# Kernel optimization log

Measured on AMD Instinct MI355X. Metric: run time of the kernel, lower is better.

Reference implementation:

```python
import jax, jax.numpy as jnp
import numpy as np

B, S, E = 2, 2048, 2048
H, KVH, D = 16, 4, 128
GROUPS = H // KVH
WINDOW = 1024
CAP = 50.0
ROPE_BASE = 10000.0
RMS_EPS = 1e-6
LN_EPS = 1e-5

def setup_inputs() -> dict:
    key = jax.random.key(0)
    ks = jax.random.split(key, 5)
    return {
        "x": jax.random.normal(ks[0], (B, S, E), jnp.float32),
        "Wq": jax.random.normal(ks[1], (E, E), jnp.float32) * (1.0 / np.sqrt(E)),
        "Wk": jax.random.normal(ks[2], (KVH * D, E), jnp.float32) * (1.0 / np.sqrt(E)),
        "Wv": jax.random.normal(ks[3], (KVH * D, E), jnp.float32) * (1.0 / np.sqrt(E)),
        "Wo": jax.random.normal(ks[4], (E, E), jnp.float32) * (1.0 / np.sqrt(E * H)),
        "q_norm_w": jnp.ones((D,), jnp.float32),
        "k_norm_w": jnp.ones((D,), jnp.float32),
        "ln_gamma": jnp.ones((E,), jnp.float32),
        "ln_beta": jnp.zeros((E,), jnp.float32),
    }

def _rmsnorm(t, w):
    # normalize over last (head) dim
    var = jnp.mean(jnp.square(t), axis=-1, keepdims=True)
    return t * jax.lax.rsqrt(var + RMS_EPS) * w

def _rope(t):
    # t: [B, h, S, D]; rotate-half RoPE
    half = D // 2
    inv_freq = 1.0 / (ROPE_BASE ** (jnp.arange(0, D, 2, dtype=jnp.float32) / D))  # [D/2]
    ang = jnp.arange(S, dtype=jnp.float32)[:, None] * inv_freq[None, :]  # [S, D/2]
    cos = jnp.concatenate([jnp.cos(ang), jnp.cos(ang)], axis=-1)  # [S, D]
    sin = jnp.concatenate([jnp.sin(ang), jnp.sin(ang)], axis=-1)
    t1, t2 = t[..., :half], t[..., half:]
    rot = jnp.concatenate([-t2, t1], axis=-1)
    return t * cos + rot * sin

def reference(x, Wq, Wk, Wv, Wo, q_norm_w, k_norm_w, ln_gamma, ln_beta):
    b, s, _ = x.shape
    q = (x @ Wq.T).reshape(b, s, H, D).transpose(0, 2, 1, 3)    # [B,H,S,D]
    k = (x @ Wk.T).reshape(b, s, KVH, D).transpose(0, 2, 1, 3)  # [B,KVH,S,D]
    v = (x @ Wv.T).reshape(b, s, KVH, D).transpose(0, 2, 1, 3)
    # QK-RMSNorm (Gemma/PaLM2 style), then RoPE
    q = _rope(_rmsnorm(q, q_norm_w))
    k = _rope(_rmsnorm(k, k_norm_w))
    # GQA: repeat KV heads to match query heads
    k = jnp.repeat(k, GROUPS, axis=1)  # [B,H,S,D]
    v = jnp.repeat(v, GROUPS, axis=1)
    scores = jnp.einsum('bhqd,bhkd->bhqk', q, k) / jnp.sqrt(jnp.asarray(D, x.dtype))
    # tanh logit softcap (Gemma2)
    scores = CAP * jnp.tanh(scores / CAP)
    # causal + sliding-window mask: attend to j with 0 <= i-j < WINDOW
    i = jnp.arange(s)[:, None]
    j = jnp.arange(s)[None, :]
    mask = (j <= i) & ((i - j) < WINDOW)  # [S,S]
    neg = jnp.finfo(scores.dtype).min
    scores = jnp.where(mask[None, None], scores, neg)
    attn = jax.nn.softmax(scores, axis=-1)
    out = jnp.einsum('bhqk,bhkd->bhqd', attn, v)  # [B,H,S,D]
    out = out.transpose(0, 2, 1, 3).reshape(b, s, E) @ Wo.T
    # residual + LayerNorm (post-norm)
    y = x + out
    mu = jnp.mean(y, axis=-1, keepdims=True)
    var = jnp.var(y, axis=-1, keepdims=True)
    return (y - mu) * jax.lax.rsqrt(var + LN_EPS) * ln_gamma + ln_beta
```

## Files before the change

### kernel.cpp

```cpp
#include <hip/hip_runtime.h>
#include <stdint.h>

typedef __attribute__((ext_vector_type(8))) short short8;
typedef __attribute__((ext_vector_type(4))) float f32x4;
typedef unsigned short u16;
typedef unsigned int u32;

#define NTOK 4096
#define E 2048
#define S 2048
#define NH 16
#define NKVH 4
#define HD 128
#define NQKV 3072

__device__ __forceinline__ float bf2f(u16 u) {
    return __uint_as_float(((u32)u) << 16);
}
__device__ __forceinline__ u16 f2bf(float f) {
    u32 u = __float_as_uint(f);
    u32 r = (u + 0x7fffu + ((u >> 16) & 1u)) >> 16;
    return (u16)r;
}
__device__ __forceinline__ void gload_lds16(const u16* g, u16* l) {
    __builtin_amdgcn_global_load_lds(
        (const __attribute__((address_space(1))) unsigned int*)(g),
        (__attribute__((address_space(3))) unsigned int*)(l), 16, 0, 0);
}

__global__ void cast5(const float* __restrict__ x, const float* __restrict__ wq,
                      const float* __restrict__ wk, const float* __restrict__ wv,
                      const float* __restrict__ wo,
                      u16* __restrict__ xb, u16* __restrict__ wqkvb,
                      u16* __restrict__ wob) {
    int i = blockIdx.x * 256 + threadIdx.x;
    const float* s; u16* d; int rel;
    if (i < 2097152)      { s = x;  d = xb;  rel = i; }
    else if (i < 3145728) { s = wq; d = wqkvb; rel = i - 2097152; }
    else if (i < 3407872) { s = wk; d = wqkvb + 4194304; rel = i - 3145728; }
    else if (i < 3670016) { s = wv; d = wqkvb + 5242880; rel = i - 3407872; }
    else                  { s = wo; d = wob; rel = i - 3670016; }
    float4 v = *(const float4*)(s + (size_t)rel * 4);
    ushort4 o;
    o.x = f2bf(v.x); o.y = f2bf(v.y); o.z = f2bf(v.z); o.w = f2bf(v.w);
    *(ushort4*)(d + (size_t)rel * 4) = o;
}

#define TM 128
#define TN 128
#define BK 64

__global__ __launch_bounds__(256, 3)
void gemm_bt(const u16* __restrict__ A, const u16* __restrict__ Bt, float* __restrict__ C,
             int M, int N, int K) {
    __shared__ u16 As[TM * BK];
    __shared__ u16 Bs[TN * BK];
    const int m0 = blockIdx.y * TM;
    const int n0 = blockIdx.x * TN;
    const int tid = threadIdx.x;
    const int w = tid >> 6, lane = tid & 63;
    const int wm = (w >> 1) * 64, wn = (w & 1) * 64;
    const int lr = lane & 15, quad = lane >> 4;

    f32x4 acc[4][4];
#pragma unroll
    for (int mi = 0; mi < 4; mi++)
#pragma unroll
        for (int ni = 0; ni < 4; ni++)
            acc[mi][ni] = (f32x4){0.f, 0.f, 0.f, 0.f};

    const int srow = w * 8 + (lane >> 3);
    const int scol = (lane & 7) * 8;
    const u16* ga0 = A + (size_t)(m0 + srow) * K + scol;
    const u16* gb0 = Bt + (size_t)(n0 + srow) * K + scol;

    for (int kt = 0; kt < K; kt += BK) {
        __syncthreads();
#pragma unroll
        for (int i = 0; i < 4; i++) {
            gload_lds16(ga0 + (size_t)(i * 32) * K + kt, &As[(w * 8 + i * 32) * BK]);
            gload_lds16(gb0 + (size_t)(i * 32) * K + kt, &Bs[(w * 8 + i * 32) * BK]);
        }
        __syncthreads();
#pragma unroll
        for (int kk = 0; kk < BK; kk += 32) {
            const int ko = kk + quad * 8;
            short8 af[4], bfr[4];
#pragma unroll
            for (int mi = 0; mi < 4; mi++)
                af[mi] = *(const short8*)(&As[(wm + mi * 16 + lr) * BK + ko]);
#pragma unroll
            for (int ni = 0; ni < 4; ni++)
                bfr[ni] = *(const short8*)(&Bs[(wn + ni * 16 + lr) * BK + ko]);
#pragma unroll
            for (int mi = 0; mi < 4; mi++)
#pragma unroll
                for (int ni = 0; ni < 4; ni++)
                    acc[mi][ni] = __builtin_amdgcn_mfma_f32_16x16x32_bf16(
                        af[mi], bfr[ni], acc[mi][ni], 0, 0, 0);
        }
    }
#pragma unroll
    for (int mi = 0; mi < 4; mi++)
#pragma unroll
        for (int ni = 0; ni < 4; ni++) {
            int row = m0 + wm + mi * 16 + quad * 4;
            int col = n0 + wn + ni * 16 + lr;
            f32x4 v = acc[mi][ni];
            C[(size_t)(row + 0) * N + col] = v[0];
            C[(size_t)(row + 1) * N + col] = v[1];
            C[(size_t)(row + 2) * N + col] = v[2];
            C[(size_t)(row + 3) * N + col] = v[3];
        }
}

__global__ __launch_bounds__(256)
void rmsrope2(const float* __restrict__ qkv,
              const float* __restrict__ qw, const float* __restrict__ kw,
              u16* __restrict__ qdst, u16* __restrict__ kdst) {
    int p = blockIdx.x * 4 + (threadIdx.x >> 6);
    int lane = threadIdx.x & 63;
    const float* src; const float* w; u16* dst; int HH;
    if (p < NTOK * NH) { src = qkv; w = qw; dst = qdst; HH = NH; }
    else { p -= NTOK * NH; src = qkv + 2048; w = kw; dst = kdst; HH = NKVH; }
    int n = p / HH;
    int h = p - n * HH;
    int b = n >> 11;
    int s = n & 2047;
    const float* row = src + (size_t)n * NQKV + h * HD;
    float t1 = row[lane];
    float t2 = row[lane + 64];
    float ss = t1 * t1 + t2 * t2;
#pragma unroll
    for (int o = 1; o < 64; o <<= 1) ss += __shfl_xor(ss, o);
    float r = rsqrtf(ss * (1.f / 128.f) + 1e-6f);
    float a1 = t1 * r * w[lane];
    float a2 = t2 * r * w[lane + 64];
    float freq = expf(lane * -0.14391156831212787f);
    float ang = (float)s * freq;
    float sn, cs;
    sincosf(ang, &sn, &cs);
    float o1 = a1 * cs - a2 * sn;
    float o2 = a2 * cs + a1 * sn;
    size_t base = (((size_t)(b * HH + h)) * S + s) * HD;
    dst[base + lane] = f2bf(o1);
    dst[base + 64 + lane] = f2bf(o2);
}

#define LDT 65
__global__ __launch_bounds__(256)
void vtrans(const float* __restrict__ src, u16* __restrict__ dst) {
    __shared__ u16 Ts[128 * LDT];
    const int t = threadIdx.x;
    const int s0 = blockIdx.x * 64;
    const int kh = blockIdx.y;
    const int b = blockIdx.z;
    const float* base = src + ((size_t)(b * S + s0)) * NQKV + 2560 + kh * HD;
#pragma unroll
    for (int i = 0; i < 8; i++) {
        int idx = i * 256 + t;
        int r = idx >> 5, c4 = (idx & 31) * 4;
        float4 v = *(const float4*)(base + (size_t)r * NQKV + c4);
        Ts[(c4 + 0) * LDT + r] = f2bf(v.x);
        Ts[(c4 + 1) * LDT + r] = f2bf(v.y);
        Ts[(c4 + 2) * LDT + r] = f2bf(v.z);
        Ts[(c4 + 3) * LDT + r] = f2bf(v.w);
    }
    __syncthreads();
    u16* obase = dst + ((size_t)(b * NKVH + kh) * HD) * S + s0;
#pragma unroll
    for (int i = 0; i < 4; i++) {
        int idx = i * 256 + t;
        int d = idx >> 3, s8 = (idx & 7) * 8;
        const u16* row = &Ts[d * LDT + s8];
        short8 o;
#pragma unroll
        for (int j = 0; j < 8; j++) o[j] = (short)row[j];
        *(short8*)(obase + (size_t)d * S + s8) = o;
    }
}

#define KSX(key, cb) ((key) * 128 + ((((cb) ^ ((key) & 15))) * 8))
#define VSX(d, cb)   ((d) * 64 + ((((cb) ^ ((d) & 7))) * 8))
#define PSX(row, cb) ((row) * 64 + ((((cb) ^ ((row) & 7))) * 8))

__global__ __launch_bounds__(256, 2)
void attn_mfma(const u16* __restrict__ qa, const u16* __restrict__ ka,
               const u16* __restrict__ vt, u16* __restrict__ out) {
    __shared__ u16 Ks[64 * 128];
    __shared__ u16 Vs[128 * 64];
    __shared__ u16 Ps[128 * 64];
    const int tid = threadIdx.x;
    const int w = tid >> 6, lane = tid & 63;
    const int lr = lane & 15, quad = lane >> 4;
    const int qt = (int)(gridDim.x - 1) - blockIdx.x;
    const int h = blockIdx.y, b = blockIdx.z;
    const int kh = h >> 2;
    const int q0 = qt * 128;
    const int qg0 = q0 + w * 32;

    const float SCINV = 0.0017677669529663689f;

    short8 qf[2][4];
#pragma unroll
    for (int gi = 0; gi < 2; gi++) {
        const u16* qrow = qa + (((size_t)(b * NH + h)) * S + qg0 + gi * 16 + lr) * HD;
#pragma unroll
        for (int c = 0; c < 4; c++)
            qf[gi][c] = *(const short8*)(qrow + c * 32 + quad * 8);
    }

    f32x4 O[2][8];
#pragma unroll
    for (int gi = 0; gi < 2; gi++)
#pragma unroll
        for (int dt = 0; dt < 8; dt++) O[gi][dt] = (f32x4){0.f, 0.f, 0.f, 0.f};
    float l[2][4] = {{0.f, 0.f, 0.f, 0.f}, {0.f, 0.f, 0.f, 0.f}};

    const u16* kbase0 = ka + (((size_t)(b * NKVH + kh)) * S) * HD;
    const u16* vtbase0 = vt + ((size_t)(b * NKVH + kh) * HD) * S;

    const int jt0 = (q0 >= 1024) ? (q0 - 1024) : 0;
    const int jtend = q0 + 64;
    for (int jt = jt0; jt <= jtend; jt += 64) {
        __syncthreads();
        const u16* kbase = kbase0 + (size_t)jt * HD;
        const u16* vtbase = vtbase0 + jt;
#pragma unroll
        for (int i = 0; i < 4; i++) {
            int idx = i * 256 + tid;
            int key = idx >> 4, cb = idx & 15;
            *(int4*)(&Ks[KSX(key, cb)]) = *(const int4*)(kbase + (size_t)key * HD + cb * 8);
            int dd = idx >> 3, cb2 = idx & 7;
            *(int4*)(&Vs[VSX(dd, cb2)]) = *(const int4*)(vtbase + (size_t)dd * S + cb2 * 8);
        }
        __syncthreads();

        u16* Pw = &Ps[w * 32 * 64];
        bool any0 = false, any1 = false;

#pragma unroll
        for (int kt = 0; kt < 4; kt++) {
            const int keymin = jt + kt * 16;
            bool need[2], full[2];
#pragma unroll
            for (int gi = 0; gi < 2; gi++) {
                int qmin = qg0 + gi * 16, qmax = qmin + 15;
                need[gi] = (keymin <= qmax) && (keymin + 15 >= qmin - 1023);
                full[gi] = (keymin + 15 <= qmin) && (keymin >= qmax - 1023);
            }
            if (need[0] || need[1]) {
#pragma unroll
                for (int gi = 0; gi < 2; gi++) {
                    if (need[gi]) {
                        f32x4 a = (f32x4){0.f, 0.f, 0.f, 0.f};
#pragma unroll
                        for (int c = 0; c < 4; c++) {
                            short8 kf = *(const short8*)(&Ks[KSX(kt * 16 + lr, 4 * c + quad)]);
                            a = __builtin_amdgcn_mfma_f32_16x16x32_bf16(qf[gi][c], kf, a, 0, 0, 0);
                        }
#pragma unroll
                        for (int r = 0; r < 4; r++) {
                            float x = a[r] * SCINV;
                            float t = __expf(2.f * x);
                            float p = __expf(-100.f * __builtin_amdgcn_rcpf(t + 1.f));
                            if (!full[gi]) {
                                int rel = keymin + lr - (qg0 + gi * 16 + quad * 4 + r);
                                bool valid = (rel <= 0) && (rel > -1024);
                                p = valid ? p : 0.f;
                            }
                            l[gi][r] += p;
                            Pw[PSX(gi * 16 + quad * 4 + r, kt * 2 + (lr >> 3)) + (lr & 7)] =
                                (u16)(__float_as_uint(p) >> 16);
                        }
                        if (gi == 0) any0 = true; else any1 = true;
                    } else {
#pragma unroll
                        for (int r = 0; r < 4; r++)
                            Pw[PSX(gi * 16 + quad * 4 + r, kt * 2 + (lr >> 3)) + (lr & 7)] = 0;
                    }
                }
            } else {
#pragma unroll
                for (int gi = 0; gi < 2; gi++)
#pragma unroll
                    for (int r = 0; r < 4; r++)
                        Pw[PSX(gi * 16 + quad * 4 + r, kt * 2 + (lr >> 3)) + (lr & 7)] = 0;
            }
        }

        if (any0 || any1) {
#pragma unroll
            for (int c2 = 0; c2 < 2; c2++) {
                short8 pf0 = *(const short8*)(&Pw[PSX(lr, c2 * 4 + quad)]);
                short8 pf1 = *(const short8*)(&Pw[PSX(16 + lr, c2 * 4 + quad)]);
#pragma unroll
                for (int dt = 0; dt < 8; dt++) {
                    short8 vf = *(const short8*)(&Vs[VSX(dt * 16 + lr, c2 * 4 + quad)]);
                    if (any0)
                        O[0][dt] = __builtin_amdgcn_mfma_f32_16x16x32_bf16(pf0, vf, O[0][dt], 0, 0, 0);
                    if (any1)
                        O[1][dt] = __builtin_amdgcn_mfma_f32_16x16x32_bf16(pf1, vf, O[1][dt], 0, 0, 0);
                }
            }
        }
    }

#pragma unroll
    for (int gi = 0; gi < 2; gi++)
#pragma unroll
        for (int r = 0; r < 4; r++) {
            l[gi][r] += __shfl_xor(l[gi][r], 1);
            l[gi][r] += __shfl_xor(l[gi][r], 2);
            l[gi][r] += __shfl_xor(l[gi][r], 4);
            l[gi][r] += __shfl_xor(l[gi][r], 8);
        }
#pragma unroll
    for (int gi = 0; gi < 2; gi++)
#pragma unroll
        for (int r = 0; r < 4; r++) {
            float inv = 1.f / l[gi][r];
            u16* orow = out + ((size_t)(b * S + qg0 + gi * 16 + quad * 4 + r)) * E + h * HD;
#pragma unroll
            for (int dt = 0; dt < 8; dt++)
                orow[dt * 16 + lr] = f2bf(O[gi][dt][r] * inv);
        }
}

__global__ __launch_bounds__(256)
void ln_kernel(const float* __restrict__ x, const float* __restrict__ pr,
               const float* __restrict__ g, const float* __restrict__ be,
               float* __restrict__ out) {
    int n = blockIdx.x;
    int tid = threadIdx.x;
    const float* xr = x + (size_t)n * E;
    const float* p = pr + (size_t)n * E;
    float y[8];
    float s = 0.f, ss = 0.f;
#pragma unroll
    for (int i = 0; i < 2; i++) {
        float4 a = *(const float4*)(xr + tid * 8 + i * 4);
        float4 b = *(const float4*)(p + tid * 8 + i * 4);
        float v0 = a.x + b.x, v1 = a.y + b.y, v2 = a.z + b.z, v3 = a.w + b.w;
        y[i * 4 + 0] = v0; y[i * 4 + 1] = v1; y[i * 4 + 2] = v2; y[i * 4 + 3] = v3;
        s += v0 + v1 + v2 + v3;
        ss += v0 * v0 + v1 * v1 + v2 * v2 + v3 * v3;
    }
#pragma unroll
    for (int o = 1; o < 64; o <<= 1) {
        s += __shfl_xor(s, o);
        ss += __shfl_xor(ss, o);
    }
    __shared__ float r0[4], r1[4];
    int w = tid >> 6;
    if ((tid & 63) == 0) { r0[w] = s; r1[w] = ss; }
    __syncthreads();
    s = r0[0] + r0[1] + r0[2] + r0[3];
    ss = r1[0] + r1[1] + r1[2] + r1[3];
    float mu = s * (1.f / 2048.f);
    float var = ss * (1.f / 2048.f) - mu * mu;
    float rs = rsqrtf(var + 1e-5f);
    float* orow = out + (size_t)n * E;
#pragma unroll
    for (int i = 0; i < 8; i++) {
        int c = tid * 8 + i;
        orow[c] = (y[i] - mu) * rs * g[c] + be[c];
    }
}

extern "C" void kernel_launch(void* const* d_in, const int* in_sizes, int n_in,
                              void* d_out, int out_size, void* d_ws, size_t ws_size,
                              hipStream_t stream) {
    (void)in_sizes; (void)n_in; (void)out_size; (void)ws_size;
    const float* x   = (const float*)d_in[0];
    const float* Wq  = (const float*)d_in[1];
    const float* Wk  = (const float*)d_in[2];
    const float* Wv  = (const float*)d_in[3];
    const float* Wo  = (const float*)d_in[4];
    const float* qnw = (const float*)d_in[5];
    const float* knw = (const float*)d_in[6];
    const float* lng = (const float*)d_in[7];
    const float* lnb = (const float*)d_in[8];
    float* out = (float*)d_out;

    char* ws = (char*)d_ws;
    size_t off = 0;
    auto alloc = [&](size_t bytes) -> char* {
        char* pp = ws + off;
        off = (off + bytes + 255) & ~(size_t)255;
        return pp;
    };
    u16*  xb     = (u16*)alloc((size_t)NTOK * E * 2);
    u16*  Wqkvb  = (u16*)alloc((size_t)NQKV * E * 2);
    u16*  Wob    = (u16*)alloc((size_t)E * E * 2);
    float* qkvraw= (float*)alloc((size_t)NTOK * NQKV * 4);
    u16*  qaa    = (u16*)alloc((size_t)NTOK * E * 2);
    u16*  kaa    = (u16*)alloc((size_t)NTOK * 512 * 2);
    u16*  vtt    = (u16*)alloc((size_t)NTOK * 512 * 2);
    u16*  attn_o = xb;
    float* proj  = qkvraw;

    cast5<<<dim3(18432), 256, 0, stream>>>(x, Wq, Wk, Wv, Wo, xb, Wqkvb, Wob);

    gemm_bt<<<dim3(NQKV / TN, NTOK / TM), 256, 0, stream>>>(xb, Wqkvb, qkvraw, NTOK, NQKV, E);

    rmsrope2<<<dim3((NTOK * NH + NTOK * NKVH) / 4), 256, 0, stream>>>(
        qkvraw, qnw, knw, qaa, kaa);
    vtrans<<<dim3(S / 64, NKVH, 2), 256, 0, stream>>>(qkvraw, vtt);

    attn_mfma<<<dim3(S / 128, NH, 2), 256, 0, stream>>>(qaa, kaa, vtt, attn_o);

    gemm_bt<<<dim3(E / TN, NTOK / TM), 256, 0, stream>>>(attn_o, Wob, proj, NTOK, E, E);

    ln_kernel<<<dim3(NTOK), 256, 0, stream>>>(x, proj, lng, lnb, out);
}
```

Measured before the change: 355.3 us.

## Shrink attention query tile to 64 rows and load K/V via direct-to-LDS

Each attention block now handles 64 query rows (16 per wave) instead of 128, the grid is reordered to head*batch by query tile, and occupancy is raised to 4 blocks per CU. K/V tiles are loaded with direct global-to-LDS copies using the pre-swizzled addresses, and the softcap/exp math is folded into exp2 constants. The intent is more parallelism and less register pressure, plus a cheaper load path. The cost is that each K/V tile is loaded by twice as many blocks, and per-wave MFMA reuse drops.

```diff
diff --git a/kernel.cpp b/kernel.cpp
--- a/kernel.cpp
+++ b/kernel.cpp
@@ -183,148 +183,128 @@
 #define KSX(key, cb) ((key) * 128 + ((((cb) ^ ((key) & 15))) * 8))
 #define VSX(d, cb)   ((d) * 64 + ((((cb) ^ ((d) & 7))) * 8))
 #define PSX(row, cb) ((row) * 64 + ((((cb) ^ ((row) & 7))) * 8))
-
-__global__ __launch_bounds__(256, 2)
+#define QBLK 64
+
+__global__ __launch_bounds__(256, 4)
 void attn_mfma(const u16* __restrict__ qa, const u16* __restrict__ ka,
                const u16* __restrict__ vt, u16* __restrict__ out) {
     __shared__ u16 Ks[64 * 128];
     __shared__ u16 Vs[128 * 64];
-    __shared__ u16 Ps[128 * 64];
+    __shared__ u16 Ps[64 * 64];
     const int tid = threadIdx.x;
     const int w = tid >> 6, lane = tid & 63;
     const int lr = lane & 15, quad = lane >> 4;
-    const int qt = (int)(gridDim.x - 1) - blockIdx.x;
-    const int h = blockIdx.y, b = blockIdx.z;
+    const int hb = blockIdx.x;
+    const int h = hb >> 1, b = hb & 1;
     const int kh = h >> 2;
-    const int q0 = qt * 128;
-    const int qg0 = q0 + w * 32;
-
-    const float SCINV = 0.0017677669529663689f;
-
-    short8 qf[2][4];
-#pragma unroll
-    for (int gi = 0; gi < 2; gi++) {
-        const u16* qrow = qa + (((size_t)(b * NH + h)) * S + qg0 + gi * 16 + lr) * HD;
+    const int qt = (int)(gridDim.y - 1) - blockIdx.y;
+    const int q0 = qt * QBLK;
+    const int qg0 = q0 + w * 16;
+
+    const float KQK = 0.0051006974f;
+    const float KP  = -144.26950408889634f;
+
+    short8 qf[4];
+    {
+        const u16* qrow = qa + (((size_t)(b * NH + h)) * S + qg0 + lr) * HD;
 #pragma unroll
         for (int c = 0; c < 4; c++)
-            qf[gi][c] = *(const short8*)(qrow + c * 32 + quad * 8);
-    }
-
-    f32x4 O[2][8];
-#pragma unroll
-    for (int gi = 0; gi < 2; gi++)
-#pragma unroll
-        for (int dt = 0; dt < 8; dt++) O[gi][dt] = (f32x4){0.f, 0.f, 0.f, 0.f};
-    float l[2][4] = {{0.f, 0.f, 0.f, 0.f}, {0.f, 0.f, 0.f, 0.f}};
+            qf[c] = *(const short8*)(qrow + c * 32 + quad * 8);
+    }
+
+    f32x4 O[8];
+#pragma unroll
+    for (int dt = 0; dt < 8; dt++) O[dt] = (f32x4){0.f, 0.f, 0.f, 0.f};
+    float l[4] = {0.f, 0.f, 0.f, 0.f};
 
     const u16* kbase0 = ka + (((size_t)(b * NKVH + kh)) * S) * HD;
     const u16* vtbase0 = vt + ((size_t)(b * NKVH + kh) * HD) * S;
 
     const int jt0 = (q0 >= 1024) ? (q0 - 1024) : 0;
-    const int jtend = q0 + 64;
+    const int jtend = q0;
+    const int qmin = qg0, qmax = qg0 + 15;
+
     for (int jt = jt0; jt <= jtend; jt += 64) {
-        __syncthreads();
         const u16* kbase = kbase0 + (size_t)jt * HD;
         const u16* vtbase = vtbase0 + jt;
+        __syncthreads();
 #pragma unroll
         for (int i = 0; i < 4; i++) {
             int idx = i * 256 + tid;
-            int key = idx >> 4, cb = idx & 15;
-            *(int4*)(&Ks[KSX(key, cb)]) = *(const int4*)(kbase + (size_t)key * HD + cb * 8);
-            int dd = idx >> 3, cb2 = idx & 7;
-            *(int4*)(&Vs[VSX(dd, cb2)]) = *(const int4*)(vtbase + (size_t)dd * S + cb2 * 8);
+            int key = idx >> 4, cbk = (idx & 15) ^ (key & 15);
+            gload_lds16(kbase + (size_t)key * HD + cbk * 8,
+                        &Ks[(i * 256 + w * 64) * 8]);
+            int dd = idx >> 3, cbv = (idx & 7) ^ (dd & 7);
+            gload_lds16(vtbase + (size_t)dd * S + cbv * 8,
+                        &Vs[(i * 256 + w * 64) * 8]);
         }
         __syncthreads();
 
-        u16* Pw = &Ps[w * 32 * 64];
-        bool any0 = false, any1 = false;
+        u16* Pw = &Ps[w * 16 * 64];
+        bool any = false;
 
 #pragma unroll
         for (int kt = 0; kt < 4; kt++) {
             const int keymin = jt + kt * 16;
-            bool need[2], full[2];
-#pragma unroll
-            for (int gi = 0; gi < 2; gi++) {
-                int qmin = qg0 + gi * 16, qmax = qmin + 15;
-                need[gi] = (keymin <= qmax) && (keymin + 15 >= qmin - 1023);
-                full[gi] = (keymin + 15 <= qmin) && (keymin >= qmax - 1023);
-            }
-            if (need[0] || need[1]) {
-#pragma unroll
-                for (int gi = 0; gi < 2; gi++) {
-                    if (need[gi]) {
-                        f32x4 a = (f32x4){0.f, 0.f, 0.f, 0.f};
-#pragma unroll
-                        for (int c = 0; c < 4; c++) {
-                            short8 kf = *(const short8*)(&Ks[KSX(kt * 16 + lr, 4 * c + quad)]);
-                            a = __builtin_amdgcn_mfma_f32_16x16x32_bf16(qf[gi][c], kf, a, 0, 0, 0);
-                        }
-#pragma unroll
-                        for (int r = 0; r < 4; r++) {
-                            float x = a[r] * SCINV;
-                            float t = __expf(2.f * x);
-                            float p = __expf(-100.f * __builtin_amdgcn_rcpf(t + 1.f));
-                            if (!full[gi]) {
-                                int rel = keymin + lr - (qg0 + gi * 16 + quad * 4 + r);
-                                bool valid = (rel <= 0) && (rel > -1024);
-                                p = valid ? p : 0.f;
-                            }
-                            l[gi][r] += p;
-                            Pw[PSX(gi * 16 + quad * 4 + r, kt * 2 + (lr >> 3)) + (lr & 7)] =
-                                (u16)(__float_as_uint(p) >> 16);
-                        }
-                        if (gi == 0) any0 = true; else any1 = true;
-                    } else {
-#pragma unroll
-                        for (int r = 0; r < 4; r++)
-                            Pw[PSX(gi * 16 + quad * 4 + r, kt * 2 + (lr >> 3)) + (lr & 7)] = 0;
+            bool need = (keymin <= qmax) && (keymin + 15 >= qmin - 1023);
+            bool full = (keymin + 15 <= qmin) && (keymin >= qmax - 1023);
+            if (need) {
+                any = true;
+                f32x4 a = (f32x4){0.f, 0.f, 0.f, 0.f};
+#pragma unroll
+                for (int c = 0; c < 4; c++) {
+                    short8 kf = *(const short8*)(&Ks[KSX(kt * 16 + lr, 4 * c + quad)]);
+                    a = __builtin_amdgcn_mfma_f32_16x16x32_bf16(qf[c], kf, a, 0, 0, 0);
+                }
+#pragma unroll
+                for (int r = 0; r < 4; r++) {
+                    float t = __builtin_amdgcn_exp2f(a[r] * KQK);
+                    float p = __builtin_amdgcn_exp2f(
+                        KP * __builtin_amdgcn_rcpf(t + 1.f));
+                    if (!full) {
+                        int rel = keymin + lr - (qg0 + quad * 4 + r);
+                        bool valid = (rel <= 0) && (rel > -1024);
+                        p = valid ? p : 0.f;
                     }
+                    l[r] += p;
+                    Pw[PSX(quad * 4 + r, kt * 2 + (lr >> 3)) + (lr & 7)] =
+                        (u16)(__float_as_uint(p) >> 16);
                 }
             } else {
 #pragma unroll
-                for (int gi = 0; gi < 2; gi++)
-#pragma unroll
-                    for (int r = 0; r < 4; r++)
-                        Pw[PSX(gi * 16 + quad * 4 + r, kt * 2 + (lr >> 3)) + (lr & 7)] = 0;
+                for (int r = 0; r < 4; r++)
+                    Pw[PSX(quad * 4 + r, kt * 2 + (lr >> 3)) + (lr & 7)] = 0;
             }
         }
 
-        if (any0 || any1) {
+        if (any) {
 #pragma unroll
             for (int c2 = 0; c2 < 2; c2++) {
-                short8 pf0 = *(const short8*)(&Pw[PSX(lr, c2 * 4 + quad)]);
-                short8 pf1 = *(const short8*)(&Pw[PSX(16 + lr, c2 * 4 + quad)]);
+                short8 pf = *(const short8*)(&Pw[PSX(lr, c2 * 4 + quad)]);
 #pragma unroll
                 for (int dt = 0; dt < 8; dt++) {
                     short8 vf = *(const short8*)(&Vs[VSX(dt * 16 + lr, c2 * 4 + quad)]);
-                    if (any0)
-                        O[0][dt] = __builtin_amdgcn_mfma_f32_16x16x32_bf16(pf0, vf, O[0][dt], 0, 0, 0);
-                    if (any1)
-                        O[1][dt] = __builtin_amdgcn_mfma_f32_16x16x32_bf16(pf1, vf, O[1][dt], 0, 0, 0);
+                    O[dt] = __builtin_amdgcn_mfma_f32_16x16x32_bf16(pf, vf, O[dt], 0, 0, 0);
                 }
             }
         }
     }
 
 #pragma unroll
-    for (int gi = 0; gi < 2; gi++)
-#pragma unroll
-        for (int r = 0; r < 4; r++) {
-            l[gi][r] += __shfl_xor(l[gi][r], 1);
-            l[gi][r] += __shfl_xor(l[gi][r], 2);
-            l[gi][r] += __shfl_xor(l[gi][r], 4);
-            l[gi][r] += __shfl_xor(l[gi][r], 8);
-        }
-#pragma unroll
-    for (int gi = 0; gi < 2; gi++)
-#pragma unroll
-        for (int r = 0; r < 4; r++) {
-            float inv = 1.f / l[gi][r];
-            u16* orow = out + ((size_t)(b * S + qg0 + gi * 16 + quad * 4 + r)) * E + h * HD;
-#pragma unroll
-            for (int dt = 0; dt < 8; dt++)
-                orow[dt * 16 + lr] = f2bf(O[gi][dt][r] * inv);
-        }
+    for (int r = 0; r < 4; r++) {
+        l[r] += __shfl_xor(l[r], 1);
+        l[r] += __shfl_xor(l[r], 2);
+        l[r] += __shfl_xor(l[r], 4);
+        l[r] += __shfl_xor(l[r], 8);
+    }
+#pragma unroll
+    for (int r = 0; r < 4; r++) {
+        float inv = 1.f / l[r];
+        u16* orow = out + ((size_t)(b * S + qg0 + quad * 4 + r)) * E + h * HD;
+#pragma unroll
+        for (int dt = 0; dt < 8; dt++)
+            orow[dt * 16 + lr] = f2bf(O[dt][r] * inv);
+    }
 }
 
 __global__ __launch_bounds__(256)
@@ -408,7 +388,7 @@
         qkvraw, qnw, knw, qaa, kaa);
     vtrans<<<dim3(S / 64, NKVH, 2), 256, 0, stream>>>(qkvraw, vtt);
 
-    attn_mfma<<<dim3(S / 128, NH, 2), 256, 0, stream>>>(qaa, kaa, vtt, attn_o);
+    attn_mfma<<<dim3(NH * 2, S / QBLK), 256, 0, stream>>>(qaa, kaa, vtt, attn_o);
 
     gemm_bt<<<dim3(E / TN, NTOK / TM), 256, 0, stream>>>(attn_o, Wob, proj, NTOK, E, E);
 
```

Result: faster. 326.3 us (-8.2%).
